# Performance work log

Hardware: AMD Instinct MI355X
Metric: run time of the kernel (lower is better)

Reference implementation:

```python
import jax, jax.numpy as jnp
import numpy as np

N = 100000
E = 3200000
IN_DIM = 512
HID = [64, 32, 16]
OUT_DIM = 40
BN_EPS = 1e-5


def setup_inputs() -> dict:
    key = jax.random.key(0)
    ks = jax.random.split(key, 10)
    x = jax.random.normal(ks[0], (N, IN_DIM), dtype=jnp.float32)
    edge_row = jnp.sort(jax.random.randint(ks[1], (E,), 0, N, dtype=jnp.int32))
    edge_col = jax.random.randint(ks[2], (E,), 0, N, dtype=jnp.int32)
    edge_val = jax.random.uniform(ks[3], (E,), dtype=jnp.float32)

    def xavier(k, fan_in, fan_out):
        limit = np.sqrt(6.0 / (fan_in + fan_out)).astype(np.float32)
        return jax.random.uniform(k, (fan_in, fan_out), dtype=jnp.float32, minval=-limit, maxval=limit)

    W1 = xavier(ks[4], IN_DIM, HID[0])
    W2 = xavier(ks[5], HID[0], HID[1])
    W3 = xavier(ks[6], HID[1], HID[2])
    W4 = xavier(ks[7], HID[2], OUT_DIM)
    return {
        "x": x, "edge_row": edge_row, "edge_col": edge_col, "edge_val": edge_val,
        "W1": W1, "W2": W2, "W3": W3, "W4": W4,
        "g1": jnp.ones((HID[0],), jnp.float32), "b1": jnp.zeros((HID[0],), jnp.float32),
        "g2": jnp.ones((HID[1],), jnp.float32), "b2": jnp.zeros((HID[1],), jnp.float32),
        "g3": jnp.ones((HID[2],), jnp.float32), "b3": jnp.zeros((HID[2],), jnp.float32),
    }


def _gcn_layer(h, W, edge_row, edge_col, edge_val, n_nodes):
    # support = h @ W  (dense GEMM), then SpMM: out[i] = sum_{e: row[e]=i} val[e] * support[col[e]]
    support = h @ W
    msgs = edge_val[:, None] * support[edge_col]  # gather + scale
    return jax.ops.segment_sum(msgs, edge_row, num_segments=n_nodes)


def _bn_elu(h, gamma, beta):
    # BatchNorm1d in training mode: batch statistics over the node dim, biased variance
    mean = jnp.mean(h, axis=0)
    var = jnp.var(h, axis=0)
    h = (h - mean) * jax.lax.rsqrt(var + BN_EPS) * gamma + beta
    return jax.nn.elu(h)


def reference(x, edge_row, edge_col, edge_val, W1, W2, W3, W4, g1, b1, g2, b2, g3, b3):
    n = x.shape[0]
    h = _gcn_layer(x, W1, edge_row, edge_col, edge_val, n)
    h = _bn_elu(h, g1, b1)  # dropout is identity in eval mode
    h = _gcn_layer(h, W2, edge_row, edge_col, edge_val, n)
    h = _bn_elu(h, g2, b2)
    h = _gcn_layer(h, W3, edge_row, edge_col, edge_val, n)
    h = _bn_elu(h, g3, b3)
    h = _gcn_layer(h, W4, edge_row, edge_col, edge_val, n)
    return jax.nn.log_softmax(h, axis=1)
```

## Files before the change

kernel.cpp:

```cpp
#include <hip/hip_runtime.h>
#include <hip/hip_bf16.h>
#include <math.h>

typedef __attribute__((ext_vector_type(8))) short short8;
typedef __attribute__((ext_vector_type(4))) float floatx4;

__global__ void rowptr_k(const int* __restrict__ erow, int* __restrict__ rp, int n, int e) {
    int i = blockIdx.x * blockDim.x + threadIdx.x;
    if (i > n) return;
    int lo = 0, hi = e;
    while (lo < hi) {
        int mid = (lo + hi) >> 1;
        if (erow[mid] < i) lo = mid + 1; else hi = mid;
    }
    rp[i] = lo;
}

__global__ void zero_k(float* __restrict__ p) {
    int i = threadIdx.x;
    if (i < 224) p[i] = 0.f;
}

__device__ __forceinline__ float elu_f(float t) {
    return t > 0.f ? t : expm1f(t);
}

__device__ __forceinline__ unsigned short f2bf(float f) {
    unsigned int u = __float_as_uint(f);
    u = (u + 0x7FFFu + ((u >> 16) & 1u)) >> 16;
    return (unsigned short)u;
}

__device__ __forceinline__ unsigned int f2bf2(float lo, float hi) {
    unsigned int a = __float_as_uint(lo);
    unsigned int b = __float_as_uint(hi);
    a = (a + 0x7FFFu + ((a >> 16) & 1u)) >> 16;
    b = (b + 0x7FFFu + ((b >> 16) & 1u)) & 0xFFFF0000u;
    return a | b;
}

__device__ __forceinline__ float bflo(unsigned int d) { return __uint_as_float(d << 16); }
__device__ __forceinline__ float bfhi(unsigned int d) { return __uint_as_float(d & 0xFFFF0000u); }

__global__ __launch_bounds__(256) void w1bf_k(const float* __restrict__ W,
                                              unsigned short* __restrict__ Wb) {
    int idx = blockIdx.x * 256 + threadIdx.x;
    int n = idx >> 9, k = idx & 511;
    Wb[idx] = f2bf(W[(long)k * 64 + n]);
}

__global__ __launch_bounds__(256) void wsmall_k(const float* __restrict__ W2,
                                                const float* __restrict__ W3,
                                                unsigned short* __restrict__ Wb2,
                                                unsigned short* __restrict__ Wb3) {
    int idx = blockIdx.x * 256 + threadIdx.x;
    if (idx < 2048) {
        int n = idx >> 6, k = idx & 63;
        Wb2[idx] = f2bf(W2[(long)k * 32 + n]);
    }
    if (idx < 512) {
        int n = idx >> 5, k = idx & 31;
        Wb3[idx] = f2bf(W3[(long)k * 16 + n]);
    }
}

__global__ __launch_bounds__(256) void gemm1_mfma_k(const float* __restrict__ X,
                                                    const unsigned short* __restrict__ Wb,
                                                    unsigned short* __restrict__ out, int nrows) {
    const int lane = threadIdx.x & 63;
    const int wid  = threadIdx.x >> 6;
    const int lrow = lane & 15;
    const int quad = lane >> 4;
    const int m0   = (blockIdx.x * 4 + wid) * 16;
    if (m0 >= nrows) return;

    int arow = m0 + lrow;
    if (arow >= nrows) arow = nrows - 1;
    const float* __restrict__ xrow = X + (long)arow * 512 + quad * 8;
    const unsigned short* __restrict__ brow = Wb + lrow * 512 + quad * 8;

    floatx4 acc[4];
#pragma unroll
    for (int ni = 0; ni < 4; ++ni) acc[ni] = (floatx4){0.f, 0.f, 0.f, 0.f};

    float4 ca0 = *(const float4*)(xrow + 0);
    float4 ca1 = *(const float4*)(xrow + 4);
    short8 cb[4];
#pragma unroll
    for (int ni = 0; ni < 4; ++ni) cb[ni] = *(const short8*)(brow + ni * 8192);

#pragma unroll
    for (int kc = 0; kc < 16; ++kc) {
        float4 na0, na1;
        short8 nb[4];
        if (kc < 15) {
            const float* xp = xrow + (kc + 1) * 32;
            na0 = *(const float4*)(xp + 0);
            na1 = *(const float4*)(xp + 4);
#pragma unroll
            for (int ni = 0; ni < 4; ++ni)
                nb[ni] = *(const short8*)(brow + ni * 8192 + (kc + 1) * 32);
        }
        union { short8 s; unsigned int u[4]; } af;
        af.u[0] = f2bf2(ca0.x, ca0.y);
        af.u[1] = f2bf2(ca0.z, ca0.w);
        af.u[2] = f2bf2(ca1.x, ca1.y);
        af.u[3] = f2bf2(ca1.z, ca1.w);
#pragma unroll
        for (int ni = 0; ni < 4; ++ni)
            acc[ni] = __builtin_amdgcn_mfma_f32_16x16x32_bf16(af.s, cb[ni], acc[ni], 0, 0, 0);
        if (kc < 15) {
            ca0 = na0; ca1 = na1;
#pragma unroll
            for (int ni = 0; ni < 4; ++ni) cb[ni] = nb[ni];
        }
    }

#pragma unroll
    for (int r = 0; r < 4; ++r) {
        int gr = m0 + quad * 4 + r;
        if (gr < nrows) {
#pragma unroll
            for (int ni = 0; ni < 4; ++ni)
                out[(long)gr * 64 + ni * 16 + lrow] = f2bf(acc[ni][r]);
        }
    }
}

template<int K, int KP, int NF, int NSTR>
__global__ __launch_bounds__(256) void gemmS_k(const unsigned short* __restrict__ H,
                                               const unsigned short* __restrict__ Wb,
                                               const float* __restrict__ stats,
                                               const float* __restrict__ gamma,
                                               const float* __restrict__ beta,
                                               unsigned short* __restrict__ out,
                                               int nrows) {
    __shared__ __align__(16) float scs[K];
    __shared__ __align__(16) float shs[K];
    const int tid = threadIdx.x;
    if (tid < K) {
        float s1 = stats[tid], s2 = stats[K + tid];
        float mean = s1 / (float)nrows;
        float var  = s2 / (float)nrows - mean * mean;
        float rstd = rsqrtf(var + 1e-5f);
        float scl  = gamma[tid] * rstd;
        scs[tid] = scl;
        shs[tid] = beta[tid] - mean * scl;
    }
    __syncthreads();

    const int lane = tid & 63;
    const int wid  = tid >> 6;
    const int lrow = lane & 15;
    const int quad = lane >> 4;
    const int m0   = (blockIdx.x * 4 + wid) * 16;
    if (m0 >= nrows) return;

    int arow = m0 + lrow;
    if (arow >= nrows) arow = nrows - 1;
    const unsigned short* __restrict__ hrow = H + (long)arow * K;

    floatx4 acc[NF];
#pragma unroll
    for (int ni = 0; ni < NF; ++ni) acc[ni] = (floatx4){0.f, 0.f, 0.f, 0.f};

#pragma unroll
    for (int kc = 0; kc < KP; kc += 32) {
        const int k8 = kc + quad * 8;
        union { short8 s; unsigned int u[4]; } af;
        if (k8 < K) {
            uint4 d = *(const uint4*)(hrow + k8);
            float4 sc0 = *(const float4*)&scs[k8];
            float4 sc1 = *(const float4*)&scs[k8 + 4];
            float4 sh0 = *(const float4*)&shs[k8];
            float4 sh1 = *(const float4*)&shs[k8 + 4];
            float f0 = elu_f(bflo(d.x) * sc0.x + sh0.x);
            float f1 = elu_f(bfhi(d.x) * sc0.y + sh0.y);
            float f2 = elu_f(bflo(d.y) * sc0.z + sh0.z);
            float f3 = elu_f(bfhi(d.y) * sc0.w + sh0.w);
            float f4 = elu_f(bflo(d.z) * sc1.x + sh1.x);
            float f5 = elu_f(bfhi(d.z) * sc1.y + sh1.y);
            float f6 = elu_f(bflo(d.w) * sc1.z + sh1.z);
            float f7 = elu_f(bfhi(d.w) * sc1.w + sh1.w);
            af.u[0] = f2bf2(f0, f1);
            af.u[1] = f2bf2(f2, f3);
            af.u[2] = f2bf2(f4, f5);
            af.u[3] = f2bf2(f6, f7);
        } else {
            af.u[0] = af.u[1] = af.u[2] = af.u[3] = 0u;
        }
#pragma unroll
        for (int ni = 0; ni < NF; ++ni) {
            short8 bf = *(const short8*)&Wb[(ni * 16 + lrow) * KP + k8];
            acc[ni] = __builtin_amdgcn_mfma_f32_16x16x32_bf16(af.s, bf, acc[ni], 0, 0, 0);
        }
    }

#pragma unroll
    for (int r = 0; r < 4; ++r) {
        int gr = m0 + quad * 4 + r;
        if (gr < nrows) {
#pragma unroll
            for (int ni = 0; ni < NF; ++ni)
                out[(long)gr * NSTR + ni * 16 + lrow] = f2bf(acc[ni][r]);
        }
    }
}

template<int F>
__global__ __launch_bounds__(256) void spmmb_k(const int* __restrict__ rp,
                                               const int* __restrict__ ecol,
                                               const float* __restrict__ ev,
                                               const unsigned short* __restrict__ sup,
                                               unsigned short* __restrict__ out, int n) {
    constexpr int GL = F / 4;
    constexpr int G  = 64 / GL;
    const int lane = threadIdx.x & 63;
    const int node = (blockIdx.x * blockDim.x + threadIdx.x) >> 6;
    if (node >= n) return;
    int s = __builtin_amdgcn_readfirstlane(rp[node]);
    int e = __builtin_amdgcn_readfirstlane(rp[node + 1]);
    const int g = lane / GL, p = lane % GL;
    float a0 = 0.f, a1 = 0.f, a2 = 0.f, a3 = 0.f;
    for (int i = s; i < e; i += 4 * G) {
#pragma unroll
        for (int b = 0; b < 4; ++b) {
            int idx = i + b * G + g;
            int cidx = idx < e ? idx : e - 1;
            int col = ecol[cidx];
            float v = ev[cidx];
            if (idx >= e) v = 0.f;
            uint2 d = *(const uint2*)((const char*)sup + (unsigned long long)col * (F * 2) + p * 8);
            a0 += v * bflo(d.x);
            a1 += v * bfhi(d.x);
            a2 += v * bflo(d.y);
            a3 += v * bfhi(d.y);
        }
    }
#pragma unroll
    for (int o = GL; o < 64; o <<= 1) {
        a0 += __shfl_xor(a0, o, 64);
        a1 += __shfl_xor(a1, o, 64);
        a2 += __shfl_xor(a2, o, 64);
        a3 += __shfl_xor(a3, o, 64);
    }
    if (lane < GL) {
        ushort4 o4;
        o4.x = f2bf(a0); o4.y = f2bf(a1); o4.z = f2bf(a2); o4.w = f2bf(a3);
        *(ushort4*)&out[(long)node * F + p * 4] = o4;
    }
}

__global__ __launch_bounds__(256) void spmmf16_k(const int* __restrict__ rp,
                                                 const int* __restrict__ ecol,
                                                 const float* __restrict__ ev,
                                                 const unsigned short* __restrict__ h,
                                                 const float* __restrict__ stats,
                                                 const float* __restrict__ gamma,
                                                 const float* __restrict__ beta,
                                                 float* __restrict__ out, int n) {
    const int lane = threadIdx.x & 63;
    const int node = (blockIdx.x * blockDim.x + threadIdx.x) >> 6;
    if (node >= n) return;
    const int g = lane >> 2, p = lane & 3;
    float scl[4], sh[4];
#pragma unroll
    for (int j = 0; j < 4; ++j) {
        int c = p * 4 + j;
        float s1 = stats[c], s2 = stats[16 + c];
        float mean = s1 / (float)n;
        float var  = s2 / (float)n - mean * mean;
        float rstd = rsqrtf(var + 1e-5f);
        scl[j] = gamma[c] * rstd;
        sh[j]  = beta[c] - mean * scl[j];
    }
    int s = __builtin_amdgcn_readfirstlane(rp[node]);
    int e = __builtin_amdgcn_readfirstlane(rp[node + 1]);
    float a0 = 0.f, a1 = 0.f, a2 = 0.f, a3 = 0.f;
    for (int i = s; i < e; i += 64) {
#pragma unroll
        for (int b = 0; b < 4; ++b) {
            int idx = i + b * 16 + g;
            int cidx = idx < e ? idx : e - 1;
            int col = ecol[cidx];
            float v = ev[cidx];
            if (idx >= e) v = 0.f;
            uint2 d = *(const uint2*)((const char*)h + (unsigned long long)col * 32 + p * 8);
            a0 += v * elu_f(bflo(d.x) * scl[0] + sh[0]);
            a1 += v * elu_f(bfhi(d.x) * scl[1] + sh[1]);
            a2 += v * elu_f(bflo(d.y) * scl[2] + sh[2]);
            a3 += v * elu_f(bfhi(d.y) * scl[3] + sh[3]);
        }
    }
#pragma unroll
    for (int o = 4; o < 64; o <<= 1) {
        a0 += __shfl_xor(a0, o, 64);
        a1 += __shfl_xor(a1, o, 64);
        a2 += __shfl_xor(a2, o, 64);
        a3 += __shfl_xor(a3, o, 64);
    }
    if (lane < 4) {
        float4 o4 = make_float4(a0, a1, a2, a3);
        *(float4*)&out[(long)node * 16 + p * 4] = o4;
    }
}

__global__ __launch_bounds__(256) void gemm4ls_k(const float* __restrict__ T,
                                                 const float* __restrict__ W4,
                                                 float* __restrict__ out, int n) {
    __shared__ __align__(16) float w[16 * 64];
    const int tid = threadIdx.x;
    for (int i = tid; i < 1024; i += 256) {
        int k = i >> 6, c = i & 63;
        w[i] = (c < 40) ? W4[k * 40 + c] : 0.f;
    }
    __syncthreads();
    const int grp = tid >> 4;
    const int p   = tid & 15;
    const int row = blockIdx.x * 16 + grp;
    if (row >= n) return;
    const float4* tp = (const float4*)(T + (long)row * 16);
    float4 t0 = tp[0], t1 = tp[1], t2 = tp[2], t3 = tp[3];
    float h[16] = {t0.x, t0.y, t0.z, t0.w, t1.x, t1.y, t1.z, t1.w,
                   t2.x, t2.y, t2.z, t2.w, t3.x, t3.y, t3.z, t3.w};
    float a0 = 0.f, a1 = 0.f, a2 = 0.f, a3 = 0.f;
#pragma unroll
    for (int k = 0; k < 16; ++k) {
        float4 wv = *(const float4*)&w[k * 64 + p * 4];
        a0 += h[k] * wv.x;
        a1 += h[k] * wv.y;
        a2 += h[k] * wv.z;
        a3 += h[k] * wv.w;
    }
    const bool valid = p < 10;
    float lm = valid ? fmaxf(fmaxf(a0, a1), fmaxf(a2, a3)) : -INFINITY;
#pragma unroll
    for (int o = 1; o < 16; o <<= 1) lm = fmaxf(lm, __shfl_xor(lm, o, 64));
    float ls = valid ? (expf(a0 - lm) + expf(a1 - lm) + expf(a2 - lm) + expf(a3 - lm)) : 0.f;
#pragma unroll
    for (int o = 1; o < 16; o <<= 1) ls += __shfl_xor(ls, o, 64);
    float lse = lm + logf(ls);
    if (valid) {
        float4 o4 = make_float4(a0 - lse, a1 - lse, a2 - lse, a3 - lse);
        *(float4*)&out[(long)row * 40 + p * 4] = o4;
    }
}

template<int F>
__global__ __launch_bounds__(256) void statsb_k(const unsigned short* __restrict__ h,
                                                float* __restrict__ stats, int n) {
    __shared__ float m1[256], m2[256], m3[256], m4[256];
    const int tid = threadIdx.x;
    const unsigned int* h2 = (const unsigned int*)h;
    const long total = (long)n * F / 2;
    float s1 = 0.f, s2 = 0.f, t1 = 0.f, t2 = 0.f;
    for (long idx = (long)blockIdx.x * 256 + tid; idx < total; idx += (long)gridDim.x * 256) {
        unsigned int d = h2[idx];
        float lo = bflo(d), hi = bfhi(d);
        s1 += lo; s2 += lo * lo;
        t1 += hi; t2 += hi * hi;
    }
    m1[tid] = s1; m2[tid] = s2; m3[tid] = t1; m4[tid] = t2;
    __syncthreads();
    if (tid < F / 2) {
#pragma unroll 4
        for (int j = 1; j < 256 / (F / 2); ++j) {
            s1 += m1[tid + j * (F / 2)];
            s2 += m2[tid + j * (F / 2)];
            t1 += m3[tid + j * (F / 2)];
            t2 += m4[tid + j * (F / 2)];
        }
        atomicAdd(&stats[2 * tid], s1);
        atomicAdd(&stats[2 * tid + 1], t1);
        atomicAdd(&stats[F + 2 * tid], s2);
        atomicAdd(&stats[F + 2 * tid + 1], t2);
    }
}

extern "C" void kernel_launch(void* const* d_in, const int* in_sizes, int n_in,
                              void* d_out, int out_size, void* d_ws, size_t ws_size,
                              hipStream_t stream) {
    const float* x    = (const float*)d_in[0];
    const int*   erow = (const int*)d_in[1];
    const int*   ecol = (const int*)d_in[2];
    const float* ev   = (const float*)d_in[3];
    const float* W1   = (const float*)d_in[4];
    const float* W2   = (const float*)d_in[5];
    const float* W3   = (const float*)d_in[6];
    const float* W4   = (const float*)d_in[7];
    const float* g1   = (const float*)d_in[8];
    const float* b1   = (const float*)d_in[9];
    const float* g2   = (const float*)d_in[10];
    const float* b2   = (const float*)d_in[11];
    const float* g3   = (const float*)d_in[12];
    const float* b3   = (const float*)d_in[13];

    const int N = in_sizes[0] / 512;
    const int E = in_sizes[1];

    char* w = (char*)d_ws;
    int* rp = (int*)w;
    size_t off = (((size_t)(N + 1) * 4) + 255) & ~(size_t)255;
    float* stats = (float*)(w + off);
    unsigned short* Abf = (unsigned short*)(stats + 256);
    unsigned short* Bbf = Abf + (size_t)N * 64;
    unsigned short* Wb1 = Bbf + (size_t)N * 64;
    unsigned short* Wb2 = Wb1 + 64 * 512;
    unsigned short* Wb3 = Wb2 + 32 * 64;
    float* Tf = (float*)Abf;
    float* outp = (float*)d_out;

    rowptr_k<<<(N + 1 + 255) / 256, 256, 0, stream>>>(erow, rp, N, E);
    zero_k<<<1, 256, 0, stream>>>(stats);
    w1bf_k<<<128, 256, 0, stream>>>(W1, Wb1);
    wsmall_k<<<8, 256, 0, stream>>>(W2, W3, Wb2, Wb3);

    const int mblocks = ((N + 15) / 16 + 3) / 4;
    const int sblocks = (N * 64 + 255) / 256;

    gemm1_mfma_k<<<mblocks, 256, 0, stream>>>(x, Wb1, Abf, N);
    spmmb_k<64><<<sblocks, 256, 0, stream>>>(rp, ecol, ev, Abf, Bbf, N);
    statsb_k<64><<<512, 256, 0, stream>>>(Bbf, stats, N);

    gemmS_k<64, 64, 2, 32><<<mblocks, 256, 0, stream>>>(Bbf, Wb2, stats, g1, b1, Abf, N);
    spmmb_k<32><<<sblocks, 256, 0, stream>>>(rp, ecol, ev, Abf, Bbf, N);
    statsb_k<32><<<512, 256, 0, stream>>>(Bbf, stats + 128, N);

    gemmS_k<32, 32, 1, 16><<<mblocks, 256, 0, stream>>>(Bbf, Wb3, stats + 128, g2, b2, Abf, N);
    spmmb_k<16><<<sblocks, 256, 0, stream>>>(rp, ecol, ev, Abf, Bbf, N);
    statsb_k<16><<<512, 256, 0, stream>>>(Bbf, stats + 192, N);

    spmmf16_k<<<sblocks, 256, 0, stream>>>(rp, ecol, ev, Bbf, stats + 192, g3, b3, Tf, N);
    gemm4ls_k<<<(N + 15) / 16, 256, 0, stream>>>(Tf, W4, outp, N);
}
```

Measured before the change: 683.6 us.

## Split small-width SpMM passes into two column-range halves for cache locality

The SpMM kernels for the 32-, 16- and final 16-wide layers now run as two passes. Each pass only gathers source rows whose column index falls in one half of the node range, so the gathered support rows should stay resident in cache. Partial sums from the first pass go to a float scratch buffer (or to the output) and are added in during the second pass. The 64-wide SpMM becomes a dedicated non-template kernel. The trade-off is that every pass re-reads the full edge list and row pointers and launches its full grid, while masked lanes still issue loads to a dummy row.

```diff
diff --git a/kernel.cpp b/kernel.cpp
--- a/kernel.cpp
+++ b/kernel.cpp
@@ -207,12 +207,55 @@
     }
 }
 
-template<int F>
-__global__ __launch_bounds__(256) void spmmb_k(const int* __restrict__ rp,
+__global__ __launch_bounds__(256) void spmm64_k(const int* __restrict__ rp,
+                                                const int* __restrict__ ecol,
+                                                const float* __restrict__ ev,
+                                                const unsigned short* __restrict__ sup,
+                                                unsigned short* __restrict__ out, int n) {
+    const int lane = threadIdx.x & 63;
+    const int node = (blockIdx.x * blockDim.x + threadIdx.x) >> 6;
+    if (node >= n) return;
+    int s = __builtin_amdgcn_readfirstlane(rp[node]);
+    int e = __builtin_amdgcn_readfirstlane(rp[node + 1]);
+    const int g = lane >> 4, p = lane & 15;
+    float a0 = 0.f, a1 = 0.f, a2 = 0.f, a3 = 0.f;
+    for (int i = s; i < e; i += 16) {
+#pragma unroll
+        for (int b = 0; b < 4; ++b) {
+            int idx = i + b * 4 + g;
+            int cidx = idx < e ? idx : e - 1;
+            int col = ecol[cidx];
+            float v = ev[cidx];
+            if (idx >= e) v = 0.f;
+            uint2 d = *(const uint2*)((const char*)sup + (unsigned long long)col * 128 + p * 8);
+            a0 += v * bflo(d.x);
+            a1 += v * bfhi(d.x);
+            a2 += v * bflo(d.y);
+            a3 += v * bfhi(d.y);
+        }
+    }
+#pragma unroll
+    for (int o = 16; o < 64; o <<= 1) {
+        a0 += __shfl_xor(a0, o, 64);
+        a1 += __shfl_xor(a1, o, 64);
+        a2 += __shfl_xor(a2, o, 64);
+        a3 += __shfl_xor(a3, o, 64);
+    }
+    if (lane < 16) {
+        ushort4 o4;
+        o4.x = f2bf(a0); o4.y = f2bf(a1); o4.z = f2bf(a2); o4.w = f2bf(a3);
+        *(ushort4*)&out[(long)node * 64 + p * 4] = o4;
+    }
+}
+
+template<int F, int PHASE>
+__global__ __launch_bounds__(256) void spmmc_k(const int* __restrict__ rp,
                                                const int* __restrict__ ecol,
                                                const float* __restrict__ ev,
                                                const unsigned short* __restrict__ sup,
-                                               unsigned short* __restrict__ out, int n) {
+                                               float* __restrict__ scr,
+                                               unsigned short* __restrict__ out,
+                                               int n, int c0, int c1) {
     constexpr int GL = F / 4;
     constexpr int G  = 64 / GL;
     const int lane = threadIdx.x & 63;
@@ -229,8 +272,10 @@
             int cidx = idx < e ? idx : e - 1;
             int col = ecol[cidx];
             float v = ev[cidx];
-            if (idx >= e) v = 0.f;
-            uint2 d = *(const uint2*)((const char*)sup + (unsigned long long)col * (F * 2) + p * 8);
+            bool keep = (idx < e) && (col >= c0) && (col < c1);
+            if (!keep) v = 0.f;
+            int gc = keep ? col : c0;
+            uint2 d = *(const uint2*)((const char*)sup + (unsigned long long)gc * (F * 2) + p * 8);
             a0 += v * bflo(d.x);
             a1 += v * bfhi(d.x);
             a2 += v * bflo(d.y);
@@ -245,20 +290,29 @@
         a3 += __shfl_xor(a3, o, 64);
     }
     if (lane < GL) {
-        ushort4 o4;
-        o4.x = f2bf(a0); o4.y = f2bf(a1); o4.z = f2bf(a2); o4.w = f2bf(a3);
-        *(ushort4*)&out[(long)node * F + p * 4] = o4;
-    }
-}
-
-__global__ __launch_bounds__(256) void spmmf16_k(const int* __restrict__ rp,
-                                                 const int* __restrict__ ecol,
-                                                 const float* __restrict__ ev,
-                                                 const unsigned short* __restrict__ h,
-                                                 const float* __restrict__ stats,
-                                                 const float* __restrict__ gamma,
-                                                 const float* __restrict__ beta,
-                                                 float* __restrict__ out, int n) {
+        long base = (long)node * F + p * 4;
+        if (PHASE == 0) {
+            *(float4*)&scr[base] = make_float4(a0, a1, a2, a3);
+        } else {
+            float4 pr = *(const float4*)&scr[base];
+            a0 += pr.x; a1 += pr.y; a2 += pr.z; a3 += pr.w;
+            ushort4 o4;
+            o4.x = f2bf(a0); o4.y = f2bf(a1); o4.z = f2bf(a2); o4.w = f2bf(a3);
+            *(ushort4*)&out[base] = o4;
+        }
+    }
+}
+
+template<int PHASE>
+__global__ __launch_bounds__(256) void spmmf16c_k(const int* __restrict__ rp,
+                                                  const int* __restrict__ ecol,
+                                                  const float* __restrict__ ev,
+                                                  const unsigned short* __restrict__ h,
+                                                  const float* __restrict__ stats,
+                                                  const float* __restrict__ gamma,
+                                                  const float* __restrict__ beta,
+                                                  float* __restrict__ out,
+                                                  int n, int c0, int c1) {
     const int lane = threadIdx.x & 63;
     const int node = (blockIdx.x * blockDim.x + threadIdx.x) >> 6;
     if (node >= n) return;
@@ -284,8 +338,10 @@
             int cidx = idx < e ? idx : e - 1;
             int col = ecol[cidx];
             float v = ev[cidx];
-            if (idx >= e) v = 0.f;
-            uint2 d = *(const uint2*)((const char*)h + (unsigned long long)col * 32 + p * 8);
+            bool keep = (idx < e) && (col >= c0) && (col < c1);
+            if (!keep) v = 0.f;
+            int gc = keep ? col : c0;
+            uint2 d = *(const uint2*)((const char*)h + (unsigned long long)gc * 32 + p * 8);
             a0 += v * elu_f(bflo(d.x) * scl[0] + sh[0]);
             a1 += v * elu_f(bfhi(d.x) * scl[1] + sh[1]);
             a2 += v * elu_f(bflo(d.y) * scl[2] + sh[2]);
@@ -300,8 +356,13 @@
         a3 += __shfl_xor(a3, o, 64);
     }
     if (lane < 4) {
-        float4 o4 = make_float4(a0, a1, a2, a3);
-        *(float4*)&out[(long)node * 16 + p * 4] = o4;
+        long base = (long)node * 16 + p * 4;
+        if (PHASE == 0) {
+            *(float4*)&out[base] = make_float4(a0, a1, a2, a3);
+        } else {
+            float4 pr = *(const float4*)&out[base];
+            *(float4*)&out[base] = make_float4(a0 + pr.x, a1 + pr.y, a2 + pr.z, a3 + pr.w);
+        }
     }
 }
 
@@ -407,6 +468,7 @@
     unsigned short* Wb1 = Bbf + (size_t)N * 64;
     unsigned short* Wb2 = Wb1 + 64 * 512;
     unsigned short* Wb3 = Wb2 + 32 * 64;
+    float* scr = (float*)((((size_t)(Wb3 + 16 * 32) + 255) & ~(size_t)255));
     float* Tf = (float*)Abf;
     float* outp = (float*)d_out;
 
@@ -417,19 +479,23 @@
 
     const int mblocks = ((N + 15) / 16 + 3) / 4;
     const int sblocks = (N * 64 + 255) / 256;
+    const int half = N / 2;
 
     gemm1_mfma_k<<<mblocks, 256, 0, stream>>>(x, Wb1, Abf, N);
-    spmmb_k<64><<<sblocks, 256, 0, stream>>>(rp, ecol, ev, Abf, Bbf, N);
+    spmm64_k<<<sblocks, 256, 0, stream>>>(rp, ecol, ev, Abf, Bbf, N);
     statsb_k<64><<<512, 256, 0, stream>>>(Bbf, stats, N);
 
     gemmS_k<64, 64, 2, 32><<<mblocks, 256, 0, stream>>>(Bbf, Wb2, stats, g1, b1, Abf, N);
-    spmmb_k<32><<<sblocks, 256, 0, stream>>>(rp, ecol, ev, Abf, Bbf, N);
+    spmmc_k<32, 0><<<sblocks, 256, 0, stream>>>(rp, ecol, ev, Abf, scr, Bbf, N, 0, half);
+    spmmc_k<32, 2><<<sblocks, 256, 0, stream>>>(rp, ecol, ev, Abf, scr, Bbf, N, half, N);
     statsb_k<32><<<512, 256, 0, stream>>>(Bbf, stats + 128, N);
 
     gemmS_k<32, 32, 1, 16><<<mblocks, 256, 0, stream>>>(Bbf, Wb3, stats + 128, g2, b2, Abf, N);
-    spmmb_k<16><<<sblocks, 256, 0, stream>>>(rp, ecol, ev, Abf, Bbf, N);
+    spmmc_k<16, 0><<<sblocks, 256, 0, stream>>>(rp, ecol, ev, Abf, scr, Bbf, N, 0, half);
+    spmmc_k<16, 2><<<sblocks, 256, 0, stream>>>(rp, ecol, ev, Abf, scr, Bbf, N, half, N);
     statsb_k<16><<<512, 256, 0, stream>>>(Bbf, stats + 192, N);
 
-    spmmf16_k<<<sblocks, 256, 0, stream>>>(rp, ecol, ev, Bbf, stats + 192, g3, b3, Tf, N);
+    spmmf16c_k<0><<<sblocks, 256, 0, stream>>>(rp, ecol, ev, Bbf, stats + 192, g3, b3, Tf, N, 0, half);
+    spmmf16c_k<2><<<sblocks, 256, 0, stream>>>(rp, ecol, ev, Bbf, stats + 192, g3, b3, Tf, N, half, N);
     gemm4ls_k<<<(N + 15) / 16, 256, 0, stream>>>(Tf, W4, outp, N);
 }
```

Result: slower. 831.1 us (+21.6%).
